# Optimization experiments

Measured on AMD Instinct MI355X. Metric: run time of the kernel, lower is better.

The kernel has to match this reference:

```python
import jax, jax.numpy as jnp
import numpy as np

D_MODEL = 1024
N_HEADS = 16
D_HEAD = D_MODEL // N_HEADS
D_FF = 4096
SEQ_LEN = 2048
BATCH = 4


def setup_inputs() -> dict:
    key = jax.random.key(0)
    ks = jax.random.split(key, 6)
    s = lambda fan_in: 1.0 / np.sqrt(fan_in)
    x = jax.random.normal(ks[0], (BATCH, SEQ_LEN, D_MODEL), dtype=jnp.float32)
    # weights stored [in, out] (transpose of torch Linear weight)
    w_qkv = jax.random.uniform(ks[1], (D_MODEL, 3 * D_MODEL), jnp.float32, -s(D_MODEL), s(D_MODEL))
    w_out = jax.random.uniform(ks[2], (D_MODEL, D_MODEL), jnp.float32, -s(D_MODEL), s(D_MODEL))
    w_ff1 = jax.random.uniform(ks[3], (D_MODEL, D_FF), jnp.float32, -s(D_MODEL), s(D_MODEL))
    w_ff2 = jax.random.uniform(ks[4], (D_FF, D_MODEL), jnp.float32, -s(D_FF), s(D_FF))
    return {"x": x, "w_qkv": w_qkv, "w_out": w_out, "w_ff1": w_ff1, "w_ff2": w_ff2}


def reference(x, w_qkv, w_out, w_ff1, w_ff2):
    B, Tlen, C = x.shape
    # ln1/ln2 are Identity (use_layer_norm=False)
    qkv = (x @ w_qkv).reshape(B, Tlen, 3, N_HEADS, D_HEAD)
    qkv = jnp.transpose(qkv, (2, 0, 3, 1, 4))  # [3, B, H, T, Dh]
    q, k, v = qkv[0], qkv[1], qkv[2]
    scale = D_HEAD ** (-0.5)
    attn = jnp.einsum("bhqd,bhkd->bhqk", q, k) * scale  # [B,H,T,T]
    causal = jnp.triu(jnp.ones((Tlen, Tlen), dtype=bool), k=1)
    attn = jnp.where(causal, -jnp.inf, attn)
    attn = jax.nn.softmax(attn, axis=-1)
    out = jnp.einsum("bhqk,bhkd->bhqd", attn, v)  # [B,H,T,Dh]
    out = jnp.transpose(out, (0, 2, 1, 3)).reshape(B, Tlen, C)
    x = x + out @ w_out
    h = jax.nn.gelu(x @ w_ff1, approximate=False)  # torch F.gelu default = exact erf
    x = x + h @ w_ff2
    return x
```

## Files before the change

kernel.cpp:

```cpp
#include <hip/hip_runtime.h>

typedef __bf16 bf16;
typedef __bf16 bf16x8 __attribute__((ext_vector_type(8)));
typedef __bf16 bf16x4 __attribute__((ext_vector_type(4)));
typedef float f32x4 __attribute__((ext_vector_type(4)));
typedef unsigned int u32;
typedef unsigned short u16;

#define MFMA_BF16 __builtin_amdgcn_mfma_f32_16x16x32_bf16

#define GLOAD_LDS(g, l)                                        \
  __builtin_amdgcn_global_load_lds(                            \
      (__attribute__((address_space(1))) void*)(g),            \
      (__attribute__((address_space(3))) void*)(l), 16, 0, 0)

__global__ void cvt_f32_bf16(const float* __restrict__ in, bf16* __restrict__ out, int n) {
  int i = (blockIdx.x * blockDim.x + threadIdx.x) * 4;
  if (i >= n) return;
  float4 v = *(const float4*)(in + i);
  bf16x4 o;
  o[0] = (bf16)v.x; o[1] = (bf16)v.y; o[2] = (bf16)v.z; o[3] = (bf16)v.w;
  *(bf16x4*)(out + i) = o;
}

__global__ void transpose_w(const float* __restrict__ w, bf16* __restrict__ wt, int K, int N) {
  __shared__ float tile[32][33];
  int n0 = blockIdx.x * 32, k0 = blockIdx.y * 32;
  int t = threadIdx.x;
  int c = t & 31, r = t >> 5;
#pragma unroll
  for (int i = 0; i < 4; i++)
    tile[r + i * 8][c] = w[(size_t)(k0 + r + i * 8) * N + n0 + c];
  __syncthreads();
#pragma unroll
  for (int i = 0; i < 4; i++)
    wt[(size_t)(n0 + r + i * 8) * K + k0 + c] = (bf16)tile[c][r + i * 8];
}

__device__ inline float gelu_exact(float x) {
  return 0.5f * x * (1.0f + erff(x * 0.70710678118654752f));
}

template <int MODE, int WTM>
__global__ __launch_bounds__(256, (WTM == 128) ? 2 : 4) void gemm_bt(
    const bf16* __restrict__ A, const bf16* __restrict__ Bt,
    bf16* __restrict__ outb, float* __restrict__ outf,
    const float* __restrict__ residf, const bf16* __restrict__ residb,
    int K, int N) {
  constexpr int BM = WTM * 2;
  constexpr int MR = WTM / 16;
  __shared__ __align__(16) bf16 As[2][BM * 32];
  __shared__ __align__(16) bf16 Bs[2][128 * 32];
  const int tid = threadIdx.x;
  const int lane = tid & 63, w = tid >> 6;
  const int g = lane >> 4, l15 = lane & 15;
  const int wm = w >> 1, wn = w & 1;

  const int NT = N >> 7;
  const int nsupN = NT >> 2;
  const int cpx = (int)gridDim.x >> 3;
  const int widx = ((int)blockIdx.x & 7) * cpx + ((int)blockIdx.x >> 3);
  const int s = widx >> 4, r4 = widx & 15;
  const int sm = s / nsupN, sn = s - sm * nsupN;
  const int m0 = (sm * 4 + (r4 & 3)) * BM;
  const int n0 = (sn * 4 + (r4 >> 2)) * 128;

  f32x4 acc[MR][4] = {};

  const int srow = tid >> 2;
  const int schunk = (tid & 3) ^ ((tid >> 3) & 3);
  const char* gA = (const char*)A;
  const char* gB = (const char*)Bt;
  const size_t aOff = ((size_t)(m0 + srow) * K + schunk * 8) * 2;
  const size_t bOff = ((size_t)(n0 + srow) * K + schunk * 8) * 2;

  auto stage = [&](int kt, int slot) {
    const size_t kb = (size_t)kt * 64;
#pragma unroll
    for (int i = 0; i < BM / 64; i++)
      GLOAD_LDS(gA + aOff + (size_t)(i * 64) * K * 2 + kb,
                &As[slot][(i * 64 + w * 16) * 32]);
#pragma unroll
    for (int i = 0; i < 2; i++)
      GLOAD_LDS(gB + bOff + (size_t)(i * 64) * K * 2 + kb,
                &Bs[slot][(i * 64 + w * 16) * 32]);
  };

  const int rsw = (g ^ ((l15 >> 1) & 3)) << 4;
  const int rdA = (wm * WTM + l15) * 64 + rsw;
  const int rdB = (wn * 64 + l15) * 64 + rsw;

  const int T = K >> 5;
  stage(0, 0);

  int slot = 0;
  for (int t = 0; t < T; ++t) {
    __syncthreads();
    if (t + 1 < T) stage(t + 1, slot ^ 1);
    const char* pA = (const char*)As[slot];
    const char* pB = (const char*)Bs[slot];
    bf16x8 a[MR], b[4];
#pragma unroll
    for (int mi = 0; mi < MR; mi++) a[mi] = *(const bf16x8*)(pA + rdA + mi * 1024);
#pragma unroll
    for (int ni = 0; ni < 4; ni++) b[ni] = *(const bf16x8*)(pB + rdB + ni * 1024);
    __builtin_amdgcn_s_setprio(1);
#pragma unroll
    for (int mi = 0; mi < MR; mi++)
#pragma unroll
      for (int ni = 0; ni < 4; ni++)
        acc[mi][ni] = MFMA_BF16(a[mi], b[ni], acc[mi][ni], 0, 0, 0);
    __builtin_amdgcn_s_setprio(0);
    slot ^= 1;
  }

  const float qsc = (MODE == 0 && n0 < 1024) ? 0.125f : 1.0f;
  const int row_base = m0 + wm * WTM;
  const int col_base = n0 + wn * 64 + l15;
#pragma unroll
  for (int mi = 0; mi < MR; mi++)
#pragma unroll
    for (int ni = 0; ni < 4; ni++) {
      const int c = col_base + ni * 16;
#pragma unroll
      for (int r = 0; r < 4; r++) {
        const int row = row_base + mi * 16 + 4 * g + r;
        const size_t idx = (size_t)row * N + c;
        float v = acc[mi][ni][r];
        if constexpr (MODE == 0) {
          outb[idx] = (bf16)(v * qsc);
        } else if constexpr (MODE == 1) {
          outb[idx] = (bf16)(v + residf[idx]);
        } else if constexpr (MODE == 2) {
          outb[idx] = (bf16)gelu_exact(v);
        } else {
          outf[idx] = v + (float)residb[idx];
        }
      }
    }
}

__global__ __launch_bounds__(512, 2) void attn_fwd(const bf16* __restrict__ qkv,
                                                   bf16* __restrict__ O) {
  __shared__ __align__(16) char Kl[2][64 * 128];
  __shared__ __align__(16) char Vt[2][64 * 128];
  const int tid = threadIdx.x;
  const int lane = tid & 63, w = tid >> 6;
  const int g = lane >> 4, l15 = lane & 15;
  const int bh = blockIdx.x;
  const int bx = blockIdx.y;
  const int b = bh >> 4, hh = bh & 15;
  const size_t tokbase = (size_t)b * 2048;

  const bf16* kbase = qkv + tokbase * 3072 + 1024 + hh * 64;
  const bf16* vbase = qkv + tokbase * 3072 + 2048 + hh * 64;
  const int kperm = 8 * (l15 >> 2) + (l15 & 3);

  const int kr8 = tid >> 3, kc = tid & 7;
  const int kswz = (kr8 & 3) | ((kr8 & 8) >> 1);
  const bf16* kSrc = kbase + (size_t)kr8 * 3072 + 8 * (kc ^ kswz);

  const bool vstage = tid < 256;
  const int t2 = tid & 255;
  const int vrg = t2 >> 4, vds = (t2 & 15) * 4;

  union U4 { ushort4 v; u16 a[4]; };
  U4 vr[4];

  auto prefetchV = [&](int k0n) {
    if (vstage) {
#pragma unroll
      for (int i4 = 0; i4 < 4; i4++)
        vr[i4].v = *(const ushort4*)(vbase + (size_t)(k0n + 4 * vrg + i4) * 3072 + vds);
    }
  };
  auto gloadK = [&](int k0n, int buf) {
    GLOAD_LDS(kSrc + (size_t)k0n * 3072, Kl[buf] + w * 1024);
  };

  prefetchV(0);
  gloadK(0, 0);
  int cur = 0;

  for (int half = 0; half < 2; half++) {
    const int xT = half ? (15 - bx) : bx;
    const int q0 = xT * 128;
    const int qw0 = q0 + 16 * w;
    const int qi = qw0 + l15;
    const int kend = q0 + 128;

    const bf16* qptr = qkv + (tokbase + qw0 + l15) * 3072 + hh * 64 + 8 * g;
    const bf16x8 qf0 = *(const bf16x8*)(qptr);
    const bf16x8 qf1 = *(const bf16x8*)(qptr + 32);

    f32x4 ot[4] = {};
    float m_i = -INFINITY, l_i = 0.0f;

    for (int k0 = 0; k0 < kend; k0 += 64) {
      char* Kc = Kl[cur];
      char* Vc = Vt[cur];
      if (vstage) {
#pragma unroll
        for (int dj = 0; dj < 4; dj++) {
          const int d = vds + dj;
          u32 lo = (u32)vr[0].a[dj] | ((u32)vr[1].a[dj] << 16);
          u32 hi2 = (u32)vr[2].a[dj] | ((u32)vr[3].a[dj] << 16);
          const int boff = d * 128 + ((((vrg >> 1) ^ ((d >> 1) & 7)) << 4)) + ((vrg & 1) << 3);
          *(uint2*)(Vc + boff) = make_uint2(lo, hi2);
        }
      }
      __syncthreads();

      const int k0n = (k0 + 64 < kend) ? k0 + 64 : 0;
      prefetchV(k0n);
      gloadK(k0n, cur ^ 1);

      if (k0 <= qw0 + 15) {
        const bool lastT = (k0 + 63 > qw0);
        const int npair = lastT ? (((qw0 + 15 - k0) >> 5) + 1) : 2;

        f32x4 st[4];
#pragma unroll
        for (int ip = 0; ip < 2; ip++)
          if (ip < npair) {
#pragma unroll
            for (int h2 = 0; h2 < 2; h2++) {
              const int kr = 32 * ip + 4 * h2 + kperm;
              const int swzk = (kr & 3) | ((kr & 8) >> 1);
              const char* kro = Kc + kr * 128;
              bf16x8 ka = *(const bf16x8*)(kro + ((g ^ swzk) << 4));
              bf16x8 kb = *(const bf16x8*)(kro + (((g | 4) ^ swzk) << 4));
              f32x4 z = {};
              z = MFMA_BF16(ka, qf0, z, 0, 0, 0);
              st[2 * ip + h2] = MFMA_BF16(kb, qf1, z, 0, 0, 0);
            }
          }

        float p[4][4];
#pragma unroll
        for (int ip = 0; ip < 2; ip++)
          if (ip < npair)
#pragma unroll
            for (int h2 = 0; h2 < 2; h2++)
#pragma unroll
              for (int r = 0; r < 4; r++)
                p[2 * ip + h2][r] = (float)st[2 * ip + h2][r];
        if (lastT) {
#pragma unroll
          for (int ip = 0; ip < 2; ip++)
            if (ip < npair)
#pragma unroll
              for (int h2 = 0; h2 < 2; h2++)
#pragma unroll
                for (int r = 0; r < 4; r++) {
                  const int kk = k0 + 32 * ip + 8 * g + 4 * h2 + r;
                  if (kk > qi) p[2 * ip + h2][r] = -INFINITY;
                }
        }
        float mt = -INFINITY;
#pragma unroll
        for (int ip = 0; ip < 2; ip++)
          if (ip < npair)
#pragma unroll
            for (int h2 = 0; h2 < 2; h2++)
#pragma unroll
              for (int r = 0; r < 4; r++) mt = fmaxf(mt, p[2 * ip + h2][r]);

        if (!__all(mt - m_i <= 8.0f)) {
          mt = fmaxf(mt, __shfl_xor(mt, 16, 64));
          mt = fmaxf(mt, __shfl_xor(mt, 32, 64));
          const float m_new = fmaxf(m_i, mt);
          const float alpha = __expf(m_i - m_new);
          l_i *= alpha;
#pragma unroll
          for (int dt = 0; dt < 4; dt++)
#pragma unroll
            for (int r = 0; r < 4; r++) ot[dt][r] *= alpha;
          m_i = m_new;
        }
        float sum = 0.0f;
#pragma unroll
        for (int ip = 0; ip < 2; ip++)
          if (ip < npair) {
#pragma unroll
            for (int h2 = 0; h2 < 2; h2++)
#pragma unroll
              for (int r = 0; r < 4; r++) {
                float e = __expf(p[2 * ip + h2][r] - m_i);
                p[2 * ip + h2][r] = e;
                sum += e;
              }
          }
        l_i += sum;

#pragma unroll
        for (int ip = 0; ip < 2; ip++)
          if (ip < npair) {
            bf16x8 pf;
#pragma unroll
            for (int h2 = 0; h2 < 2; h2++)
#pragma unroll
              for (int r = 0; r < 4; r++) pf[4 * h2 + r] = (bf16)p[2 * ip + h2][r];
#pragma unroll
            for (int dt = 0; dt < 4; dt++) {
              const bf16x8 vf = *(const bf16x8*)(
                  Vc + (dt * 16 + l15) * 128 + (((4 * ip + g) ^ (l15 >> 1)) << 4));
              ot[dt] = MFMA_BF16(vf, pf, ot[dt], 0, 0, 0);
            }
          }
      }
      cur ^= 1;
    }

    l_i += __shfl_xor(l_i, 16, 64);
    l_i += __shfl_xor(l_i, 32, 64);
    const float inv = 1.0f / l_i;
    bf16* obase = O + (tokbase + qw0 + l15) * 1024 + hh * 64;
#pragma unroll
    for (int dt = 0; dt < 4; dt++) {
      bf16x4 ov;
#pragma unroll
      for (int r = 0; r < 4; r++) ov[r] = (bf16)(ot[dt][r] * inv);
      *(bf16x4*)(obase + dt * 16 + 4 * g) = ov;
    }
  }
}

extern "C" void kernel_launch(void* const* d_in, const int* in_sizes, int n_in,
                              void* d_out, int out_size, void* d_ws, size_t ws_size,
                              hipStream_t stream) {
  const float* x = (const float*)d_in[0];
  const float* w_qkv = (const float*)d_in[1];
  const float* w_out = (const float*)d_in[2];
  const float* w_ff1 = (const float*)d_in[3];
  const float* w_ff2 = (const float*)d_in[4];
  float* out = (float*)d_out;

  char* ws = (char*)d_ws;
  size_t off = 0;
  auto alloc = [&](size_t bytes) {
    void* p = ws + off;
    off += (bytes + 255) & ~(size_t)255;
    return p;
  };
  const size_t M = 8192;
  bf16* X16   = (bf16*)alloc(M * 1024 * 2);
  bf16* WqkvT = (bf16*)alloc(3072ull * 1024 * 2);
  bf16* WoutT = (bf16*)alloc(1024ull * 1024 * 2);
  bf16* Wff1T = (bf16*)alloc(4096ull * 1024 * 2);
  bf16* Wff2T = (bf16*)alloc(1024ull * 4096 * 2);
  bf16* QKV   = (bf16*)alloc(M * 3072 * 2);
  bf16* Obuf  = (bf16*)alloc(M * 1024 * 2);
  bf16* x1b   = (bf16*)alloc(M * 1024 * 2);
  bf16* Hbuf  = (bf16*)alloc(M * 4096 * 2);

  cvt_f32_bf16<<<8192, 256, 0, stream>>>(x, X16, 8192 * 1024);
  transpose_w<<<dim3(3072 / 32, 1024 / 32), 256, 0, stream>>>(w_qkv, WqkvT, 1024, 3072);
  transpose_w<<<dim3(1024 / 32, 1024 / 32), 256, 0, stream>>>(w_out, WoutT, 1024, 1024);
  transpose_w<<<dim3(4096 / 32, 1024 / 32), 256, 0, stream>>>(w_ff1, Wff1T, 1024, 4096);
  transpose_w<<<dim3(1024 / 32, 4096 / 32), 256, 0, stream>>>(w_ff2, Wff2T, 4096, 1024);

  gemm_bt<0, 128><<<32 * 24, 256, 0, stream>>>(X16, WqkvT, QKV, nullptr, nullptr, nullptr, 1024, 3072);
  attn_fwd<<<dim3(64, 8), 512, 0, stream>>>(QKV, Obuf);
  gemm_bt<1, 64><<<64 * 8, 256, 0, stream>>>(Obuf, WoutT, x1b, nullptr, x, nullptr, 1024, 1024);
  gemm_bt<2, 128><<<32 * 32, 256, 0, stream>>>(x1b, Wff1T, Hbuf, nullptr, nullptr, nullptr, 1024, 4096);
  gemm_bt<3, 64><<<64 * 8, 256, 0, stream>>>(Hbuf, Wff2T, nullptr, out, nullptr, x1b, 4096, 1024);
}
```

Baseline: 380.4 us.

## Use single-buffered 128x128 GEMM tiles with uniform template and occupancy 3

Drops the double-buffered LDS prefetch in the GEMM kernel and replaces it with a single buffer: each k-step now stages, syncs, then computes. Tile height is unified to 128 rows for all four GEMMs, with more blocks launched for the QKV and FF1 GEMMs, and launch bounds are set to 3 waves per SIMD. This halves LDS use to allow higher occupancy, but it removes the overlap of global loads with MFMA compute and adds a second barrier per iteration.

After: 358.0 us. 1.06x faster.

```diff
diff --git a/kernel.cpp b/kernel.cpp
--- a/kernel.cpp
+++ b/kernel.cpp
@@ -41,16 +41,14 @@
   return 0.5f * x * (1.0f + erff(x * 0.70710678118654752f));
 }
 
-template <int MODE, int WTM>
-__global__ __launch_bounds__(256, (WTM == 128) ? 2 : 4) void gemm_bt(
+template <int MODE>
+__global__ __launch_bounds__(256, 3) void gemm_bt(
     const bf16* __restrict__ A, const bf16* __restrict__ Bt,
     bf16* __restrict__ outb, float* __restrict__ outf,
     const float* __restrict__ residf, const bf16* __restrict__ residb,
     int K, int N) {
-  constexpr int BM = WTM * 2;
-  constexpr int MR = WTM / 16;
-  __shared__ __align__(16) bf16 As[2][BM * 32];
-  __shared__ __align__(16) bf16 Bs[2][128 * 32];
+  __shared__ __align__(16) bf16 As[128 * 32];
+  __shared__ __align__(16) bf16 Bs[128 * 32];
   const int tid = threadIdx.x;
   const int lane = tid & 63, w = tid >> 6;
   const int g = lane >> 4, l15 = lane & 15;
@@ -62,10 +60,10 @@
   const int widx = ((int)blockIdx.x & 7) * cpx + ((int)blockIdx.x >> 3);
   const int s = widx >> 4, r4 = widx & 15;
   const int sm = s / nsupN, sn = s - sm * nsupN;
-  const int m0 = (sm * 4 + (r4 & 3)) * BM;
+  const int m0 = (sm * 4 + (r4 & 3)) * 128;
   const int n0 = (sn * 4 + (r4 >> 2)) * 128;
 
-  f32x4 acc[MR][4] = {};
+  f32x4 acc[4][4] = {};
 
   const int srow = tid >> 2;
   const int schunk = (tid & 3) ^ ((tid >> 3) & 3);
@@ -74,51 +72,48 @@
   const size_t aOff = ((size_t)(m0 + srow) * K + schunk * 8) * 2;
   const size_t bOff = ((size_t)(n0 + srow) * K + schunk * 8) * 2;
 
-  auto stage = [&](int kt, int slot) {
+  auto stage = [&](int kt) {
     const size_t kb = (size_t)kt * 64;
 #pragma unroll
-    for (int i = 0; i < BM / 64; i++)
+    for (int i = 0; i < 2; i++)
       GLOAD_LDS(gA + aOff + (size_t)(i * 64) * K * 2 + kb,
-                &As[slot][(i * 64 + w * 16) * 32]);
+                &As[(i * 64 + w * 16) * 32]);
 #pragma unroll
     for (int i = 0; i < 2; i++)
       GLOAD_LDS(gB + bOff + (size_t)(i * 64) * K * 2 + kb,
-                &Bs[slot][(i * 64 + w * 16) * 32]);
+                &Bs[(i * 64 + w * 16) * 32]);
   };
 
   const int rsw = (g ^ ((l15 >> 1) & 3)) << 4;
-  const int rdA = (wm * WTM + l15) * 64 + rsw;
+  const int rdA = (wm * 64 + l15) * 64 + rsw;
   const int rdB = (wn * 64 + l15) * 64 + rsw;
 
   const int T = K >> 5;
-  stage(0, 0);
-
-  int slot = 0;
   for (int t = 0; t < T; ++t) {
     __syncthreads();
-    if (t + 1 < T) stage(t + 1, slot ^ 1);
-    const char* pA = (const char*)As[slot];
-    const char* pB = (const char*)Bs[slot];
-    bf16x8 a[MR], b[4];
-#pragma unroll
-    for (int mi = 0; mi < MR; mi++) a[mi] = *(const bf16x8*)(pA + rdA + mi * 1024);
+    stage(t);
+    __syncthreads();
+    const char* pA = (const char*)As;
+    const char* pB = (const char*)Bs;
+    bf16x8 a[4], b[4];
+#pragma unroll
+    for (int mi = 0; mi < 4; mi++) a[mi] = *(const bf16x8*)(pA + rdA + mi * 1024);
 #pragma unroll
     for (int ni = 0; ni < 4; ni++) b[ni] = *(const bf16x8*)(pB + rdB + ni * 1024);
     __builtin_amdgcn_s_setprio(1);
 #pragma unroll
-    for (int mi = 0; mi < MR; mi++)
+    for (int mi = 0; mi < 4; mi++)
 #pragma unroll
       for (int ni = 0; ni < 4; ni++)
         acc[mi][ni] = MFMA_BF16(a[mi], b[ni], acc[mi][ni], 0, 0, 0);
     __builtin_amdgcn_s_setprio(0);
-    slot ^= 1;
   }
 
   const float qsc = (MODE == 0 && n0 < 1024) ? 0.125f : 1.0f;
-  const int row_base = m0 + wm * WTM;
+  const int row_base = m0 + wm * 64;
   const int col_base = n0 + wn * 64 + l15;
 #pragma unroll
-  for (int mi = 0; mi < MR; mi++)
+  for (int mi = 0; mi < 4; mi++)
 #pragma unroll
     for (int ni = 0; ni < 4; ni++) {
       const int c = col_base + ni * 16;
@@ -360,9 +355,9 @@
   transpose_w<<<dim3(4096 / 32, 1024 / 32), 256, 0, stream>>>(w_ff1, Wff1T, 1024, 4096);
   transpose_w<<<dim3(1024 / 32, 4096 / 32), 256, 0, stream>>>(w_ff2, Wff2T, 4096, 1024);
 
-  gemm_bt<0, 128><<<32 * 24, 256, 0, stream>>>(X16, WqkvT, QKV, nullptr, nullptr, nullptr, 1024, 3072);
+  gemm_bt<0><<<64 * 24, 256, 0, stream>>>(X16, WqkvT, QKV, nullptr, nullptr, nullptr, 1024, 3072);
   attn_fwd<<<dim3(64, 8), 512, 0, stream>>>(QKV, Obuf);
-  gemm_bt<1, 64><<<64 * 8, 256, 0, stream>>>(Obuf, WoutT, x1b, nullptr, x, nullptr, 1024, 1024);
-  gemm_bt<2, 128><<<32 * 32, 256, 0, stream>>>(x1b, Wff1T, Hbuf, nullptr, nullptr, nullptr, 1024, 4096);
-  gemm_bt<3, 64><<<64 * 8, 256, 0, stream>>>(Hbuf, Wff2T, nullptr, out, nullptr, x1b, 4096, 1024);
-}
+  gemm_bt<1><<<64 * 8, 256, 0, stream>>>(Obuf, WoutT, x1b, nullptr, x, nullptr, 1024, 1024);
+  gemm_bt<2><<<64 * 32, 256, 0, stream>>>(x1b, Wff1T, Hbuf, nullptr, nullptr, nullptr, 1024, 4096);
+  gemm_bt<3><<<64 * 8, 256, 0, stream>>>(Hbuf, Wff2T, nullptr, out, nullptr, x1b, 4096, 1024);
+}
```
